# Performance work log

Measured on AMD Instinct MI355X. Metric: run time of the kernel, lower is better.

Reference implementation:

```python
import jax, jax.numpy as jnp
import numpy as np
from jax.scipy.special import gammaln

# NQ_IN + 4 == 2*H is required because the two kernel=1, padding=1 convs grow the
# length axis by 4 and the following nn.Linear(2H, H) acts on the length axis.
B, NQ_IN, NK, QDIM, KDIM, H = 16, 2044, 1024, 80, 256, 1024


def setup_inputs() -> dict:
    ks = jax.random.split(jax.random.key(0), 14)
    s = 0.02
    return {
        "query": jax.random.normal(ks[0], (B, NQ_IN, QDIM), jnp.float32),
        "key": jax.random.normal(ks[1], (B, NK, KDIM), jnp.float32),
        "query_lens": jnp.full((B,), 2 * H, jnp.int32),
        "key_lens": jnp.full((B,), NK, jnp.int32),
        # query branch params (Conv1d k=1 stored as (out,in); Linear as (out,in))
        "qc1_w": jax.random.normal(ks[2], (2 * H, QDIM), jnp.float32) * s,
        "qc1_b": jax.random.normal(ks[3], (2 * H,), jnp.float32) * s,
        "qc2_w": jax.random.normal(ks[4], (2 * H, 2 * H), jnp.float32) * s,
        "qc2_b": jax.random.normal(ks[5], (2 * H,), jnp.float32) * s,
        "ql_w": jax.random.normal(ks[6], (H, 2 * H), jnp.float32) * s,
        "ql_b": jax.random.normal(ks[7], (H,), jnp.float32) * s,
        # key branch params
        "kc_w": jax.random.normal(ks[8], (H, KDIM, 3), jnp.float32) * s,
        "kc_b": jax.random.normal(ks[9], (H,), jnp.float32) * s,
        "kl1_w": jax.random.normal(ks[10], (2 * H, H), jnp.float32) * s,
        "kl1_b": jax.random.normal(ks[11], (2 * H,), jnp.float32) * s,
        "kl2_w": jax.random.normal(ks[12], (H, 2 * H), jnp.float32) * s,
        "kl2_b": jax.random.normal(ks[13], (H,), jnp.float32) * s,
    }


def _log_beta_binom(query_lens, key_lens, tq, tk):
    # Standard MAS beta-binomial alignment prior over a (tq, tk) grid.
    i = jnp.arange(tq, dtype=jnp.float32)[None, :, None]
    j = jnp.arange(tk, dtype=jnp.float32)[None, None, :]
    ql = query_lens.astype(jnp.float32)[:, None, None]
    kl = key_lens.astype(jnp.float32)[:, None, None]
    a = i + 1.0
    b = jnp.maximum(ql - i, 1.0)
    n = jnp.maximum(kl - 1.0, 0.0)
    nmj = jnp.maximum(n - j, 0.0)

    def betaln(x, y):
        return gammaln(x) + gammaln(y) - gammaln(x + y)

    logp = (gammaln(n + 1.0) - gammaln(j + 1.0) - gammaln(nmj + 1.0)
            + betaln(j + a, nmj + b) - betaln(a, b))
    valid = (i < ql) & (j < kl)
    return jnp.where(valid, logp, -1e9)


def _forward(query, key, query_lens, key_lens,
             qc1_w, qc1_b, qc2_w, qc2_b, ql_w, ql_b,
             kc_w, kc_b, kl1_w, kl1_b, kl2_w, kl2_b):
    # query branch: b n c -> b c n, two k=1/p=1 convs (pad length, pointwise), Linear over LENGTH axis
    q = jnp.transpose(query, (0, 2, 1))                       # (B, QDIM, NQ_IN)
    q = jnp.pad(q, ((0, 0), (0, 0), (1, 1)))
    q = jnp.einsum('bcn,oc->bon', q, qc1_w) + qc1_b[None, :, None]   # (B, 2H, NQ_IN+2)
    q = jnp.pad(q, ((0, 0), (0, 0), (1, 1)))
    q = jnp.einsum('bcn,oc->bon', q, qc2_w) + qc2_b[None, :, None]   # (B, 2H, 2H)
    q = jnp.einsum('bcn,hn->bch', q, ql_w) + ql_b                    # (B, 2H, H) Linear on length axis

    # key branch: b n c -> b c n, Conv1d k=3 p=1, then two Linears over LENGTH axis
    k = jnp.transpose(key, (0, 2, 1))                         # (B, KDIM, NK)
    k = jax.lax.conv_general_dilated(k, kc_w, (1,), ((1, 1),),
                                     dimension_numbers=('NCH', 'OIH', 'NCH'))
    k = k + kc_b[None, :, None]                               # (B, H, NK=H)
    k = jnp.einsum('bcn,on->bco', k, kl1_w) + kl1_b           # (B, H, 2H)
    k = jnp.einsum('bco,ho->bch', k, kl2_w) + kl2_b           # (B, H, H)

    # dist = -cdist(q, k), computed via the GEMM form (same as torch.cdist mm mode)
    sq = (jnp.sum(q * q, -1)[:, :, None] + jnp.sum(k * k, -1)[:, None, :]
          - 2.0 * jnp.einsum('bnd,bmd->bnm', q, k))           # (B, 2H, H)
    dist = -jnp.sqrt(jnp.maximum(sq, 1e-12))

    prior = _log_beta_binom(query_lens, key_lens, q.shape[1], k.shape[1])
    return jax.nn.log_softmax(dist + prior, axis=-1)


def reference(query, key, query_lens, key_lens,
              qc1_w, qc1_b, qc2_w, qc2_b, ql_w, ql_b,
              kc_w, kc_b, kl1_w, kl1_b, kl2_w, kl2_b):
    return _forward(query, key, query_lens, key_lens,
                    qc1_w, qc1_b, qc2_w, qc2_b, ql_w, ql_b,
                    kc_w, kc_b, kl1_w, kl1_b, kl2_w, kl2_b)
```

## Files before the change

### kernel.cpp

```cpp
#include <hip/hip_runtime.h>
#include <math.h>

typedef unsigned short u16;
typedef float floatx4 __attribute__((ext_vector_type(4)));
typedef __bf16 bf16x8 __attribute__((ext_vector_type(8)));

#define BB   16
#define TQ   2048
#define TK   1024
#define HH   1024
#define H2   2048
#define QD   80
#define QDP  128
#define KD   256
#define NQ   2044
#define NKEY 1024
#define T12N 3072

__device__ __forceinline__ u16 f2bf(float f) {
  unsigned int u = __float_as_uint(f);
  u = u + 0x7fffu + ((u >> 16) & 1u);
  return (u16)(u >> 16);
}
__device__ __forceinline__ float bf2f(u16 s) {
  return __uint_as_float(((unsigned int)s) << 16);
}
__device__ __forceinline__ float tgf(const float* __restrict__ tbl, int x) {
  return tbl[(x < 8191) ? (x < 0 ? 0 : x) : 8191];
}

__global__ __launch_bounds__(256) void prep_all_k(
    const float* __restrict__ qc2_w, const float* __restrict__ kl2_w,
    const float* __restrict__ ql_w, const float* __restrict__ kc_w,
    const float* __restrict__ kl1_w,
    u16* __restrict__ qc2w, u16* __restrict__ kl2w, u16* __restrict__ qlw2,
    u16* __restrict__ kcp, float* __restrict__ colsum1, float* __restrict__ tbl)
{
  long b = blockIdx.x;
  const int t = threadIdx.x;
  __shared__ float red[256];
  if (b < 16384) {
    long i = b * 256 + t; qc2w[i] = f2bf(qc2_w[i]); return;
  }
  b -= 16384;
  if (b < 8192) {
    long i = b * 256 + t; kl2w[i] = f2bf(kl2_w[i]); return;
  }
  b -= 8192;
  if (b < 8192) {
    long i = b * 256 + t;
    int n = (int)(i & 2047);
    int h = (int)(i >> 11);
    qlw2[i] = (n < NQ) ? f2bf(ql_w[(long)h * H2 + n + 2]) : (u16)0; return;
  }
  b -= 8192;
  if (b < 3072) {
    long i = b * 256 + t;
    int r = (int)(i % 768);
    int o = (int)(i / 768);
    int tt = r >> 8, d = r & 255;
    kcp[i] = f2bf(kc_w[((long)o * KD + d) * 3 + tt]); return;
  }
  b -= 3072;
  if (b < 2048) {
    const float* row = kl1_w + b * (long)HH;
    float s = row[t] + row[t + 256] + row[t + 512] + row[t + 768];
    red[t] = s; __syncthreads();
    for (int st = 128; st > 0; st >>= 1) { if (t < st) red[t] += red[t + st]; __syncthreads(); }
    if (!t) colsum1[b] = red[0];
    return;
  }
  b -= 2048;
  { int i = (int)(b * 256 + t); if (i < 8192) tbl[i] = i ? (float)lgamma((double)i) : 0.0f; }
}

__global__ __launch_bounds__(256) void tpack_k(
    const float* __restrict__ kl1_w, const float* __restrict__ qc1_w,
    const float* __restrict__ query,
    u16* __restrict__ kl1T, u16* __restrict__ qc1T, u16* __restrict__ qT)
{
  __shared__ float tile[64][65];
  int bid = blockIdx.x;
  const int tid = threadIdx.x;
  const int r4 = tid >> 6, c = tid & 63;
  const float* src; u16* dst;
  int sr0, sc0, srcR, srcC, srcStride, dstC;
  if (bid < 512) {
    sr0 = (bid >> 4) * 64; sc0 = (bid & 15) * 64;
    src = kl1_w; srcR = 2048; srcC = 1024; srcStride = 1024;
    dst = kl1T; dstC = 2048;
  } else if ((bid -= 512) < 64) {
    sr0 = (bid >> 1) * 64; sc0 = (bid & 1) * 64;
    src = qc1_w; srcR = 2048; srcC = QD; srcStride = QD;
    dst = qc1T; dstC = 2048;
  } else {
    bid -= 64;
    const int b16 = bid >> 6, r = bid & 63;
    sr0 = (r >> 1) * 64; sc0 = (r & 1) * 64;
    src = query + (long)b16 * NQ * QD; srcR = NQ; srcC = QD; srcStride = QD;
    dst = qT + (long)b16 * QDP * 2048; dstC = 2048;
  }
#pragma unroll
  for (int rr = r4; rr < 64; rr += 4) {
    const int gr = sr0 + rr, gc = sc0 + c;
    tile[rr][c] = (gr < srcR && gc < srcC) ? src[(long)gr * srcStride + gc] : 0.f;
  }
  __syncthreads();
#pragma unroll
  for (int rr = r4; rr < 64; rr += 4)
    dst[(long)(sc0 + rr) * dstC + sr0 + c] = f2bf(tile[c][rr]);
}

__global__ __launch_bounds__(256) void pack_kcolT_k(const float* __restrict__ key, u16* __restrict__ out) {
  __shared__ float tile[64][65];
  const int bid = blockIdx.x, tid = threadIdx.x;
  const int b = bid >> 6, r = bid & 63;
  const int m0 = (r >> 2) * 64;
  const int d0 = (r & 3) * 64;
  const int r4 = tid >> 6, c = tid & 63;
#pragma unroll
  for (int rr = r4; rr < 64; rr += 4)
    tile[rr][c] = key[((long)b * NKEY + m0 + rr) * KD + d0 + c];
  __syncthreads();
#pragma unroll
  for (int t = 0; t < 3; t++) {
    const int n = m0 + 1 - t + c;
    if (n >= 0 && n < NKEY) {
#pragma unroll
      for (int rr = r4; rr < 64; rr += 4)
        out[((long)b * 768 + t * 256 + d0 + rr) * NKEY + n] = f2bf(tile[c][rr]);
    }
  }
  if (m0 == 0 && c == 0) {
#pragma unroll
    for (int rr = r4; rr < 64; rr += 4)
      out[((long)b * 768 + d0 + rr) * NKEY + 0] = (u16)0;
  }
  if (m0 == 960 && c == 0) {
#pragma unroll
    for (int rr = r4; rr < 64; rr += 4)
      out[((long)b * 768 + 512 + d0 + rr) * NKEY + (NKEY - 1)] = (u16)0;
  }
}

__global__ __launch_bounds__(256) void fold_bias_k(
    const float* __restrict__ qc2_w, const float* __restrict__ qc1_b, const float* __restrict__ qc2_b,
    const float* __restrict__ kl2_w, const float* __restrict__ kl1_b, const float* __restrict__ kl2_b,
    const float* __restrict__ ql_w, const float* __restrict__ colsum1,
    float* __restrict__ bqm, float* __restrict__ bkv, float* __restrict__ s1v, float* __restrict__ s0v,
    float* __restrict__ wsum)
{
  const int bid = blockIdx.x, t = threadIdx.x;
  float s = 0.f, s2 = 0.f;
  if (bid < H2) {
    const float* row = qc2_w + (long)bid * H2;
    for (int k = t; k < H2; k += 256) s += row[k] * qc1_b[k];
  } else if (bid < H2 + HH) {
    const float* row = kl2_w + (long)(bid - H2) * H2;
    for (int k = t; k < H2; k += 256) { const float rv = row[k]; s += rv * kl1_b[k]; s2 += rv * colsum1[k]; }
  } else {
    const float* row = ql_w + (long)(bid - H2 - HH) * H2;
    for (int m = 1 + t; m <= H2 - 2; m += 256) s += row[m];
  }
  __shared__ float red[256];
  __shared__ float red2[256];
  red[t] = s; red2[t] = s2; __syncthreads();
  for (int st = 128; st > 0; st >>= 1) {
    if (t < st) { red[t] += red[t + st]; red2[t] += red2[t + st]; }
    __syncthreads();
  }
  if (!t) {
    if (bid < H2) bqm[bid] = red[0] + qc2_b[bid];
    else if (bid < H2 + HH) { bkv[bid - H2] = red[0] + kl2_b[bid - H2]; wsum[bid - H2] = red2[0]; }
    else {
      int h = bid - H2 - HH;
      s1v[h] = red[0];
      s0v[h] = ql_w[(long)h * H2] + ql_w[(long)h * H2 + H2 - 1];
    }
  }
}

__device__ __forceinline__ void gld_lds16(const u16* g, u16* l) {
  __builtin_amdgcn_global_load_lds((const __attribute__((address_space(1))) void*)g,
                                   (__attribute__((address_space(3))) void*)l, 16, 0, 0);
}

template<int MODE>
__global__ __launch_bounds__(256) void gemm_bt(
    const u16* __restrict__ A, const u16* __restrict__ B, void* __restrict__ Cv,
    int M, int N, int K, int lda, int ldb, int swap, int kspl,
    long sA, long sB, long sC, long sN,
    const float* __restrict__ colb, const float* __restrict__ rowb,
    const float* __restrict__ r1m, const float* __restrict__ r1n,
    const float* __restrict__ r2m, const float* __restrict__ r2n,
    const float* __restrict__ c1p, const float* __restrict__ qnp,
    const float* __restrict__ knp, const float* __restrict__ crowp,
    const float* __restrict__ t12p,
    const int* __restrict__ qlensp, const int* __restrict__ klensp)
{
  __shared__ __align__(16) u16 As[128 * 32];
  __shared__ __align__(16) u16 Bs[128 * 32];
  const int bz = blockIdx.z;
  const int bb_ = (kspl > 1) ? bz / kspl : bz;
  const int ks_ = (kspl > 1) ? bz - bb_ * kspl : 0;
  const int tid  = threadIdx.x;
  const int lane = tid & 63;
  const int wv = tid >> 6;
  const int wm = ((tid >> 7) & 1) * 64;
  const int wn = ((tid >> 6) & 1) * 64;
  const int m0 = (swap ? blockIdx.x : blockIdx.y) * 128;
  const int n0 = (swap ? blockIdx.y : blockIdx.x) * 128;

  const int srow = wv * 32 + (lane >> 2);
  const int scol = (lane & 3) << 3;
  const u16* ga = A + bb_ * sA + (long)ks_ * K + (long)(m0 + srow) * lda + scol;
  const u16* gb = B + bb_ * sB + (long)ks_ * K + (long)(n0 + srow) * ldb + scol;
  u16* la0 = &As[(wv * 32) * 32];
  u16* la1 = &As[(wv * 32 + 16) * 32];
  u16* lb0 = &Bs[(wv * 32) * 32];
  u16* lb1 = &Bs[(wv * 32 + 16) * 32];
  const long a16 = (long)16 * lda;
  const long b16 = (long)16 * ldb;

  floatx4 acc[4][4];
#pragma unroll
  for (int a_ = 0; a_ < 4; a_++)
#pragma unroll
    for (int b_ = 0; b_ < 4; b_++) acc[a_][b_] = (floatx4){0.f, 0.f, 0.f, 0.f};

  const int fr = lane & 15;
  const int fk = (lane >> 4) << 3;

  for (int kb = 0; kb < K; kb += 32) {
    gld_lds16(ga,       la0);
    gld_lds16(ga + a16, la1);
    gld_lds16(gb,       lb0);
    gld_lds16(gb + b16, lb1);
    ga += 32; gb += 32;
    __syncthreads();
    bf16x8 af[4], bfr[4];
#pragma unroll
    for (int mi = 0; mi < 4; mi++)
      af[mi] = *reinterpret_cast<const bf16x8*>(&As[(wm + mi * 16 + fr) * 32 + fk]);
#pragma unroll
    for (int ni = 0; ni < 4; ni++)
      bfr[ni] = *reinterpret_cast<const bf16x8*>(&Bs[(wn + ni * 16 + fr) * 32 + fk]);
#pragma unroll
    for (int mi = 0; mi < 4; mi++)
#pragma unroll
      for (int ni = 0; ni < 4; ni++)
        acc[mi][ni] = __builtin_amdgcn_mfma_f32_16x16x32_bf16(af[mi], bfr[ni], acc[mi][ni], 0, 0, 0);
    __syncthreads();
  }

  const int fr4 = (lane >> 4) << 2;
  const int fc  = lane & 15;
  u16*   Cb16 = (u16*)Cv + (long)bz * sC;
  float* Cb32 = (float*)Cv + (long)bz * sC;
  const float* cbp  = colb ? colb + (long)bb_ * sN : nullptr;
  const float* r1np = r1n ? r1n + (long)bb_ * sN : nullptr;
  const float* r2np = r2n ? r2n + (long)bb_ * sN : nullptr;
  int qlv = 0, klv = 0;
  if (MODE == 2) { qlv = qlensp[bb_]; klv = klensp[bb_]; }
#pragma unroll
  for (int mi = 0; mi < 4; mi++) {
#pragma unroll
    for (int ni = 0; ni < 4; ni++) {
      const int gm0 = m0 + wm + mi * 16 + fr4;
      const int gn  = n0 + wn + ni * 16 + fc;
      const float cbv  = cbp ? cbp[gn] : 0.f;
      const float r1nv = r1np ? r1np[gn] : 0.f;
      const float r2nv = r2np ? r2np[gn] : 0.f;
      float knj = 0.f, c1j = 0.f;
      union { float4 v4; float a[4]; } qn4, cr4;
      if (MODE == 2) {
        knj = knp[(long)bb_ * TK + gn];
        c1j = c1p[(long)bb_ * TK + gn];
        qn4.v4 = *reinterpret_cast<const float4*>(qnp + (long)bb_ * TQ + gm0);
        cr4.v4 = *reinterpret_cast<const float4*>(crowp + (long)bb_ * TQ + gm0);
      }
#pragma unroll
      for (int rr = 0; rr < 4; rr++) {
        const int gm = gm0 + rr;
        float v = acc[mi][ni][rr] + cbv;
        if (rowb) v += rowb[gm];
        if (r1m)  v += r1m[gm] * r1nv;
        if (r2m)  v += r2m[gm] * r2nv;
        if (MODE == 2) {
          const float sq = fmaxf(qn4.a[rr] + knj - 2.0f * v, 1e-12f);
          const float dist = -sqrtf(sq);
          float res = -1e9f;
          if (gm < qlv && gn < klv)
            res = dist + cr4.a[rr] - c1j + t12p[(long)bb_ * T12N + gm + gn];
          Cb32[(long)gm * N + gn] = res;
        }
        else if (MODE == 1) Cb32[(long)gm * N + gn] = v;
        else                Cb16[(long)gm * N + gn] = f2bf(v);
      }
    }
  }
}

__global__ __launch_bounds__(256) void reduce_bk_k(const float* __restrict__ P, u16* __restrict__ out,
                                                   long chunk, int S, long total) {
  long j = ((long)blockIdx.x * 256 + threadIdx.x) * 4;
  if (j >= total) return;
  long b = j / chunk;
  const float* p = P + j + b * chunk * (S - 1);
  float4 s = *reinterpret_cast<const float4*>(p);
  for (int t = 1; t < S; t++) {
    const float4 v = *reinterpret_cast<const float4*>(p + (long)t * chunk);
    s.x += v.x; s.y += v.y; s.z += v.z; s.w += v.w;
  }
  union { u16 h[4]; uint2 u; } o;
  o.h[0] = f2bf(s.x); o.h[1] = f2bf(s.y); o.h[2] = f2bf(s.z); o.h[3] = f2bf(s.w);
  *reinterpret_cast<uint2*>(out + j) = o.u;
}

__global__ __launch_bounds__(256) void u_k(
    const u16* __restrict__ TpT, const float* __restrict__ qlb,
    const float* __restrict__ s1, const float* __restrict__ s0,
    const float* __restrict__ tbl, const int* __restrict__ qlens, const int* __restrict__ klens,
    float* __restrict__ u0, float* __restrict__ u1, float* __restrict__ u2,
    float* __restrict__ sc, float* __restrict__ c1,
    float* __restrict__ crow, float* __restrict__ t12)
{
  const int bid = blockIdx.x, t = threadIdx.x;
  __shared__ float4 red[256];
  if (bid < BB * QDP) {
    uint2 v = reinterpret_cast<const uint2*>(TpT + (long)bid * HH)[t];
    float a0 = bf2f((u16)(v.x & 0xffff)), a1 = bf2f((u16)(v.x >> 16));
    float a2 = bf2f((u16)(v.y & 0xffff)), a3 = bf2f((u16)(v.y >> 16));
    float4 q  = reinterpret_cast<const float4*>(qlb)[t];
    float4 w1 = reinterpret_cast<const float4*>(s1)[t];
    float4 w0 = reinterpret_cast<const float4*>(s0)[t];
    float4 s;
    s.x = a0 * q.x  + a1 * q.y  + a2 * q.z  + a3 * q.w;
    s.y = a0 * w1.x + a1 * w1.y + a2 * w1.z + a3 * w1.w;
    s.z = a0 * w0.x + a1 * w0.y + a2 * w0.z + a3 * w0.w;
    s.w = 0.f;
    red[t] = s; __syncthreads();
    for (int st = 128; st > 0; st >>= 1) {
      if (t < st) { red[t].x += red[t + st].x; red[t].y += red[t + st].y; red[t].z += red[t + st].z; }
      __syncthreads();
    }
    if (!t) { u0[bid] = red[0].x; u1[bid] = red[0].y; u2[bid] = red[0].z; }
  } else if (bid < BB * QDP + 6) {
    const int idx = bid - BB * QDP;
    const float* X = (idx == 1 || idx == 5) ? s1 : (idx == 2) ? s0 : qlb;
    const float* Y = (idx == 1 || idx == 3) ? s1 : (idx == 0) ? qlb : s0;
    float4 x = reinterpret_cast<const float4*>(X)[t];
    float4 y = reinterpret_cast<const float4*>(Y)[t];
    float4 s; s.x = x.x * y.x + x.y * y.y + x.z * y.z + x.w * y.w; s.y = s.z = s.w = 0.f;
    red[t] = s; __syncthreads();
    for (int st = 128; st > 0; st >>= 1) {
      if (t < st) red[t].x += red[t + st].x;
      __syncthreads();
    }
    if (!t) sc[idx] = red[0].x;
  } else if (bid < BB * QDP + 6 + 64) {
    const int idx = bid - (BB * QDP + 6);
    const int b = idx >> 2;
    const int j = ((idx & 3) << 8) | t;
    const int kl = klens[b];
    const int n_ = (kl - 1 > 0) ? kl - 1 : 0;
    c1[b * TK + j] = tgf(tbl, j + 1) + tgf(tbl, n_ - j + 1);
  } else if (bid < BB * QDP + 6 + 64 + 128) {
    const int idx = bid - (BB * QDP + 6 + 64);
    const int b = idx >> 3;
    const int i = ((idx & 7) << 8) | t;
    const int ql = qlens[b], kl = klens[b];
    const int n_ = (kl - 1 > 0) ? kl - 1 : 0;
    const int bb = (ql - i > 1) ? ql - i : 1;
    crow[b * TQ + i] = tgf(tbl, n_ + 1) + tgf(tbl, i + 1 + bb) - tgf(tbl, i + 1)
                     - tgf(tbl, bb) - tgf(tbl, i + 1 + n_ + bb);
  } else {
    const int idx = bid - (BB * QDP + 6 + 64 + 128);
    const int b = idx / 12;
    const int s = (idx - b * 12) * 256 + t;
    const int ql = qlens[b], kl = klens[b];
    const int n_ = (kl - 1 > 0) ? kl - 1 : 0;
    t12[b * T12N + s] = tgf(tbl, s + 1) + tgf(tbl, n_ + ql - s);
  }
}

__global__ __launch_bounds__(256) void qn_k(
    const u16* __restrict__ Wq, const float* __restrict__ WqG,
    const float* __restrict__ u0, const float* __restrict__ u1, const float* __restrict__ u2,
    const float* __restrict__ bqm, const float* __restrict__ qc2_b,
    const float* __restrict__ sc, float* __restrict__ qn)
{
  const int bx = blockIdx.x, t = threadIdx.x;
  const int b = bx >> 10;
  const int i = ((bx & 1023) << 1) | (t >> 7);
  const int d = t & 127;
  const float w  = bf2f(Wq[(long)i * QDP + d]);
  const float g  = WqG[((long)b * H2 + i) * QDP + d];
  const float bq = bqm[i], q2 = qc2_b[i];
  const float uu = u0[b * QDP + d] + bq * u1[b * QDP + d] + q2 * u2[b * QDP + d];
  __shared__ float red[256];
  red[t] = w * (g + 2.f * uu); __syncthreads();
  for (int s = 64; s > 0; s >>= 1) { if ((t & 127) < s) red[t] += red[t + s]; __syncthreads(); }
  if (d == 0) {
    const float cst = sc[0] + bq * bq * sc[1] + q2 * q2 * sc[2]
                    + 2.f * (bq * sc[3] + q2 * sc[4] + bq * q2 * sc[5]);
    qn[b * TQ + i] = red[t] + cst;
  }
}

__global__ __launch_bounds__(256) void rownormk_k(
    const u16* __restrict__ K3, const float* __restrict__ qlb,
    const float* __restrict__ s1, const float* __restrict__ s0,
    float* __restrict__ kn, float* __restrict__ yb, float* __restrict__ y1, float* __restrict__ y0)
{
  const long r = blockIdx.x;
  const int t = threadIdx.x;
  uint2 v = reinterpret_cast<const uint2*>(K3 + r * HH)[t];
  float a0 = bf2f((u16)(v.x & 0xffff)), a1 = bf2f((u16)(v.x >> 16));
  float a2 = bf2f((u16)(v.y & 0xffff)), a3 = bf2f((u16)(v.y >> 16));
  float4 q  = reinterpret_cast<const float4*>(qlb)[t];
  float4 w1 = reinterpret_cast<const float4*>(s1)[t];
  float4 w0 = reinterpret_cast<const float4*>(s0)[t];
  float4 s;
  s.x = a0 * a0   + a1 * a1   + a2 * a2   + a3 * a3;
  s.y = a0 * q.x  + a1 * q.y  + a2 * q.z  + a3 * q.w;
  s.z = a0 * w1.x + a1 * w1.y + a2 * w1.z + a3 * w1.w;
  s.w = a0 * w0.x + a1 * w0.y + a2 * w0.z + a3 * w0.w;
  __shared__ float4 red[256];
  red[t] = s; __syncthreads();
  for (int st = 128; st > 0; st >>= 1) {
    if (t < st) {
      red[t].x += red[t + st].x; red[t].y += red[t + st].y;
      red[t].z += red[t + st].z; red[t].w += red[t + st].w;
    }
    __syncthreads();
  }
  if (!t) { kn[r] = red[0].x; yb[r] = red[0].y; y1[r] = red[0].z; y0[r] = red[0].w; }
}

__global__ __launch_bounds__(256) void finalize_k(float* __restrict__ out)
{
  const int i = blockIdx.x;
  const int b = blockIdx.y;
  const int tid = threadIdx.x;
  const long rowoff = ((long)b * TQ + i) * TK;
  float4 v = *reinterpret_cast<const float4*>(out + rowoff + (tid << 2));
  float m = fmaxf(fmaxf(v.x, v.y), fmaxf(v.z, v.w));
#pragma unroll
  for (int k = 1; k < 64; k <<= 1) m = fmaxf(m, __shfl_xor(m, k, 64));
  __shared__ float wred[8];
  if ((tid & 63) == 0) wred[tid >> 6] = m;
  __syncthreads();
  const float gmax = fmaxf(fmaxf(wred[0], wred[1]), fmaxf(wred[2], wred[3]));
  const float L2E = 1.4426950408889634f;
  float ls = exp2f((v.x - gmax) * L2E) + exp2f((v.y - gmax) * L2E)
           + exp2f((v.z - gmax) * L2E) + exp2f((v.w - gmax) * L2E);
#pragma unroll
  for (int k = 1; k < 64; k <<= 1) ls += __shfl_xor(ls, k, 64);
  if ((tid & 63) == 0) wred[4 + (tid >> 6)] = ls;
  __syncthreads();
  const float tot = (wred[4] + wred[5]) + (wred[6] + wred[7]);
  const float lse = gmax + logf(tot);
  v.x -= lse; v.y -= lse; v.z -= lse; v.w -= lse;
  *reinterpret_cast<float4*>(out + rowoff + (tid << 2)) = v;
}

extern "C" void kernel_launch(void* const* d_in, const int* in_sizes, int n_in,
                              void* d_out, int out_size, void* d_ws, size_t ws_size,
                              hipStream_t stream)
{
  (void)in_sizes; (void)n_in; (void)out_size; (void)ws_size;
  const float* query = (const float*)d_in[0];
  const float* key   = (const float*)d_in[1];
  const int*   qlens = (const int*)d_in[2];
  const int*   klens = (const int*)d_in[3];
  const float* qc1_w = (const float*)d_in[4];
  const float* qc1_b = (const float*)d_in[5];
  const float* qc2_w = (const float*)d_in[6];
  const float* qc2_b = (const float*)d_in[7];
  const float* ql_w  = (const float*)d_in[8];
  const float* ql_b  = (const float*)d_in[9];
  const float* kc_w  = (const float*)d_in[10];
  const float* kc_b  = (const float*)d_in[11];
  const float* kl1_w = (const float*)d_in[12];
  const float* kl1_b = (const float*)d_in[13];
  const float* kl2_w = (const float*)d_in[14];
  const float* kl2_b = (const float*)d_in[15];

  size_t off = 0;
  char* ws = (char*)d_ws;
  auto alloc = [&](size_t bytes) -> char* {
    char* p = ws + off; off += (bytes + 255) & ~(size_t)255; return p;
  };
  u16* qc2w_bf = (u16*)alloc(2ull * H2 * H2);
  u16* qc1T_bf = (u16*)alloc(2ull * QDP * H2);
  u16* kl2w_bf = (u16*)alloc(2ull * HH * H2);
  u16* kl1T_bf = (u16*)alloc(2ull * HH * H2);
  u16* qT_bf   = (u16*)alloc(2ull * BB * QDP * 2048);
  u16* kcolT_bf= (u16*)d_ws;
  u16* Z2_bf   = (u16*)d_ws;
  u16* qlw2_bf = (u16*)alloc(2ull * HH * 2048);
  u16* kcp_bf  = (u16*)alloc(2ull * HH * 768);
  u16* TpT_bf  = (u16*)alloc(2ull * H2 * HH);
  char* pool   = alloc(2ull * BB * HH * NKEY);
  float* Pbuf  = (float*)pool;
  u16* X_bf    = (u16*)pool;
  float* tbl  = (float*)alloc(4ull * 8192);
  u16* Wq_bf  = (u16*)alloc(2ull * H2 * QDP);
  u16* Wk_bf  = (u16*)alloc(2ull * HH * NKEY);
  float* bqm  = (float*)alloc(4ull * H2);
  float* bkv  = (float*)alloc(4ull * HH);
  float* s1v  = (float*)alloc(4ull * HH);
  float* s0v  = (float*)alloc(4ull * HH);
  float* wsum = (float*)alloc(4ull * HH);
  float* colsum1 = (float*)alloc(4ull * H2);
  u16* K3_bf  = (u16*)alloc(2ull * BB * TK * HH);
  float* qnv  = (float*)alloc(4ull * BB * TQ);
  float* knv  = (float*)alloc(4ull * BB * TK);
  float* ybv  = (float*)alloc(4ull * BB * TK);
  float* y1v  = (float*)alloc(4ull * BB * TK);
  float* y0v  = (float*)alloc(4ull * BB * TK);
  float* u0v  = (float*)alloc(4ull * BB * QDP);
  float* u1v  = (float*)alloc(4ull * BB * QDP);
  float* u2v  = (float*)alloc(4ull * BB * QDP);
  float* c1v  = (float*)alloc(4ull * BB * TK);
  float* crowv= (float*)alloc(4ull * BB * TQ);
  float* t12v = (float*)alloc(4ull * BB * T12N);
  float* scv  = (float*)alloc(256);
  float* WqG  = (float*)d_out;
  u16* G_bf   = (u16*)((char*)d_out + 16777216);

  prep_all_k<<<37920, 256, 0, stream>>>(qc2_w, kl2_w, ql_w, kc_w, kl1_w,
                                        qc2w_bf, kl2w_bf, qlw2_bf, kcp_bf, colsum1, tbl);
  tpack_k<<<1600, 256, 0, stream>>>(kl1_w, qc1_w, query, kl1T_bf, qc1T_bf, qT_bf);
  fold_bias_k<<<4096, 256, 0, stream>>>(qc2_w, qc1_b, qc2_b, kl2_w, kl1_b, kl2_b, ql_w, colsum1,
                                        bqm, bkv, s1v, s0v, wsum);

  gemm_bt<1><<<dim3(1, 16, 16), 256, 0, stream>>>(qc2w_bf, qc1T_bf, Pbuf, H2, QDP, 128,
      H2, H2, 0, 16, 0, 0, (long)H2 * QDP, 0,
      nullptr, nullptr, nullptr, nullptr, nullptr, nullptr,
      nullptr, nullptr, nullptr, nullptr, nullptr, nullptr, nullptr);
  reduce_bk_k<<<256, 256, 0, stream>>>(Pbuf, Wq_bf, (long)H2 * QDP, 16, (long)H2 * QDP);

  gemm_bt<1><<<dim3(8, 8, 8), 256, 0, stream>>>(kl2w_bf, kl1T_bf, Pbuf, HH, NKEY, 256,
      H2, H2, 0, 8, 0, 0, (long)HH * NKEY, 0,
      nullptr, nullptr, nullptr, nullptr, nullptr, nullptr,
      nullptr, nullptr, nullptr, nullptr, nullptr, nullptr, nullptr);
  reduce_bk_k<<<1024, 256, 0, stream>>>(Pbuf, Wk_bf, (long)HH * NKEY, 8, (long)HH * NKEY);

  gemm_bt<1><<<dim3(8, 16, 4), 256, 0, stream>>>(qT_bf, qlw2_bf, Pbuf, H2, HH, 512,
      2048, 2048, 0, 4, 0, 0, (long)H2 * HH, 0,
      nullptr, nullptr, nullptr, nullptr, nullptr, nullptr,
      nullptr, nullptr, nullptr, nullptr, nullptr, nullptr, nullptr);
  reduce_bk_k<<<2048, 256, 0, stream>>>(Pbuf, TpT_bf, (long)H2 * HH, 4, (long)H2 * HH);

  gemm_bt<1><<<dim3(1, 1, 128), 256, 0, stream>>>(TpT_bf, TpT_bf, Pbuf, 128, 128, 128,
      HH, HH, 0, 8, (long)QDP * HH, (long)QDP * HH, 128 * 128, 0,
      nullptr, nullptr, nullptr, nullptr, nullptr, nullptr,
      nullptr, nullptr, nullptr, nullptr, nullptr, nullptr, nullptr);
  reduce_bk_k<<<256, 256, 0, stream>>>(Pbuf, G_bf, 128 * 128, 8, (long)BB * 128 * 128);

  gemm_bt<1><<<dim3(1, 16, 16), 256, 0, stream>>>(Wq_bf, G_bf, WqG, H2, QDP, QDP,
      QDP, QDP, 0, 1, 0, (long)QDP * QDP, (long)H2 * QDP, 0,
      nullptr, nullptr, nullptr, nullptr, nullptr, nullptr,
      nullptr, nullptr, nullptr, nullptr, nullptr, nullptr, nullptr);
  u_k<<<BB * QDP + 6 + 64 + 128 + 192, 256, 0, stream>>>(TpT_bf, ql_b, s1v, s0v, tbl, qlens, klens,
                                                         u0v, u1v, u2v, scv, c1v, crowv, t12v);
  qn_k<<<BB * TQ / 2, 256, 0, stream>>>(Wq_bf, WqG, u0v, u1v, u2v, bqm, qc2_b, scv, qnv);

  pack_kcolT_k<<<1024, 256, 0, stream>>>(key, kcolT_bf);
  gemm_bt<0><<<dim3(6, 8, BB), 256, 0, stream>>>(Wk_bf, kcolT_bf, X_bf, HH, 768, NKEY,
      NKEY, NKEY, 0, 1, 0, (long)768 * NKEY, (long)HH * 768, 0,
      nullptr, nullptr, nullptr, nullptr, nullptr, nullptr,
      nullptr, nullptr, nullptr, nullptr, nullptr, nullptr, nullptr);
  gemm_bt<0><<<dim3(8, 8, BB), 256, 0, stream>>>(kcp_bf, X_bf, K3_bf, HH, NKEY, 768,
      768, 768, 1, 1, 0, (long)HH * 768, (long)TK * HH, 0,
      bkv, nullptr, kc_b, wsum, nullptr, nullptr,
      nullptr, nullptr, nullptr, nullptr, nullptr, nullptr, nullptr);

  gemm_bt<1><<<dim3(8, 1, 32), 256, 0, stream>>>(K3_bf, TpT_bf, Pbuf, TK, QDP, 512,
      HH, HH, 1, 2, (long)TK * HH, (long)QDP * HH, (long)TK * QDP, 0,
      nullptr, nullptr, nullptr, nullptr, nullptr, nullptr,
      nullptr, nullptr, nullptr, nullptr, nullptr, nullptr, nullptr);
  reduce_bk_k<<<2048, 256, 0, stream>>>(Pbuf, Z2_bf, (long)TK * QDP, 2, (long)BB * TK * QDP);

  rownormk_k<<<BB * TK, 256, 0, stream>>>(K3_bf, ql_b, s1v, s0v, knv, ybv, y1v, y0v);

  gemm_bt<2><<<dim3(8, 16, BB), 256, 0, stream>>>(Wq_bf, Z2_bf, (float*)d_out, H2, TK, QDP,
      QDP, QDP, 0, 1, 0, (long)TK * QDP, (long)TQ * TK, (long)TK,
      ybv, nullptr, bqm, y1v, qc2_b, y0v,
      c1v, qnv, knv, crowv, t12v, qlens, klens);

  finalize_k<<<dim3(TQ, BB, 1), 256, 0, stream>>>((float*)d_out);
}
```

Measured before the change: 650.9 us.

## Fuse distance GEMM with log-softmax using two-pass recompute in one kernel

Replaces the final MFMA GEMM epilogue kernel plus the separate row log-softmax pass with one kernel. Each block owns 128 query rows and computes the K=128 GEMM twice: first to accumulate an online max/sum-exp per row, then to write normalized outputs staged through LDS for coalesced float4 stores. This removes writing the 128MB fp32 intermediate and reading it back, at the cost of doubling the small GEMM. The grid is now only 256 blocks of 512 threads, so occupancy and parallelism are reduced.

After: 616.8 us. -5.2%, faster.

```diff
diff --git a/kernel.cpp b/kernel.cpp
--- a/kernel.cpp
+++ b/kernel.cpp
@@ -185,18 +185,14 @@
                                    (__attribute__((address_space(3))) void*)l, 16, 0, 0);
 }
 
-template<int MODE>
+template<int OUTF32>
 __global__ __launch_bounds__(256) void gemm_bt(
     const u16* __restrict__ A, const u16* __restrict__ B, void* __restrict__ Cv,
     int M, int N, int K, int lda, int ldb, int swap, int kspl,
     long sA, long sB, long sC, long sN,
     const float* __restrict__ colb, const float* __restrict__ rowb,
     const float* __restrict__ r1m, const float* __restrict__ r1n,
-    const float* __restrict__ r2m, const float* __restrict__ r2n,
-    const float* __restrict__ c1p, const float* __restrict__ qnp,
-    const float* __restrict__ knp, const float* __restrict__ crowp,
-    const float* __restrict__ t12p,
-    const int* __restrict__ qlensp, const int* __restrict__ klensp)
+    const float* __restrict__ r2m, const float* __restrict__ r2n)
 {
   __shared__ __align__(16) u16 As[128 * 32];
   __shared__ __align__(16) u16 Bs[128 * 32];
@@ -260,8 +256,6 @@
   const float* cbp  = colb ? colb + (long)bb_ * sN : nullptr;
   const float* r1np = r1n ? r1n + (long)bb_ * sN : nullptr;
   const float* r2np = r2n ? r2n + (long)bb_ * sN : nullptr;
-  int qlv = 0, klv = 0;
-  if (MODE == 2) { qlv = qlensp[bb_]; klv = klensp[bb_]; }
 #pragma unroll
   for (int mi = 0; mi < 4; mi++) {
 #pragma unroll
@@ -271,14 +265,6 @@
       const float cbv  = cbp ? cbp[gn] : 0.f;
       const float r1nv = r1np ? r1np[gn] : 0.f;
       const float r2nv = r2np ? r2np[gn] : 0.f;
-      float knj = 0.f, c1j = 0.f;
-      union { float4 v4; float a[4]; } qn4, cr4;
-      if (MODE == 2) {
-        knj = knp[(long)bb_ * TK + gn];
-        c1j = c1p[(long)bb_ * TK + gn];
-        qn4.v4 = *reinterpret_cast<const float4*>(qnp + (long)bb_ * TQ + gm0);
-        cr4.v4 = *reinterpret_cast<const float4*>(crowp + (long)bb_ * TQ + gm0);
-      }
 #pragma unroll
       for (int rr = 0; rr < 4; rr++) {
         const int gm = gm0 + rr;
@@ -286,16 +272,8 @@
         if (rowb) v += rowb[gm];
         if (r1m)  v += r1m[gm] * r1nv;
         if (r2m)  v += r2m[gm] * r2nv;
-        if (MODE == 2) {
-          const float sq = fmaxf(qn4.a[rr] + knj - 2.0f * v, 1e-12f);
-          const float dist = -sqrtf(sq);
-          float res = -1e9f;
-          if (gm < qlv && gn < klv)
-            res = dist + cr4.a[rr] - c1j + t12p[(long)bb_ * T12N + gm + gn];
-          Cb32[(long)gm * N + gn] = res;
-        }
-        else if (MODE == 1) Cb32[(long)gm * N + gn] = v;
-        else                Cb16[(long)gm * N + gn] = f2bf(v);
+        if (OUTF32) Cb32[(long)gm * N + gn] = v;
+        else        Cb16[(long)gm * N + gn] = f2bf(v);
       }
     }
   }
@@ -438,31 +416,175 @@
   if (!t) { kn[r] = red[0].x; yb[r] = red[0].y; y1[r] = red[0].z; y0[r] = red[0].w; }
 }
 
-__global__ __launch_bounds__(256) void finalize_k(float* __restrict__ out)
-{
-  const int i = blockIdx.x;
-  const int b = blockIdx.y;
-  const int tid = threadIdx.x;
-  const long rowoff = ((long)b * TQ + i) * TK;
-  float4 v = *reinterpret_cast<const float4*>(out + rowoff + (tid << 2));
-  float m = fmaxf(fmaxf(v.x, v.y), fmaxf(v.z, v.w));
-#pragma unroll
-  for (int k = 1; k < 64; k <<= 1) m = fmaxf(m, __shfl_xor(m, k, 64));
-  __shared__ float wred[8];
-  if ((tid & 63) == 0) wred[tid >> 6] = m;
+#define L2E 1.4426950408889634f
+__global__ __launch_bounds__(512) void smax_k(
+    const u16* __restrict__ Wq, const u16* __restrict__ Z2, float* __restrict__ out,
+    const float* __restrict__ ybv, const float* __restrict__ y1v, const float* __restrict__ y0v,
+    const float* __restrict__ bqmv, const float* __restrict__ qc2_b,
+    const float* __restrict__ qnv, const float* __restrict__ knv, const float* __restrict__ c1v,
+    const float* __restrict__ crowv, const float* __restrict__ t12v,
+    const int* __restrict__ qlens, const int* __restrict__ klens)
+{
+  __shared__ float vst[64][132];
+  __shared__ float t12s[1152];
+  __shared__ float qns[128], crs[128], bqms[128], q2bs[128];
+  __shared__ float2 lseb[4][128];
+  __shared__ float lsef[128];
+
+  const int mt = blockIdx.x, b = blockIdx.y;
+  const int m0 = mt * 128;
+  const int t = threadIdx.x;
+  const int w = t >> 6, lane = t & 63;
+  const int wm2 = (w >> 2) * 64, wn2 = (w & 3) * 32;
+  const int fr = lane & 15, fk = (lane >> 4) << 3;
+  const int fr4 = (lane >> 4) << 2, fc = lane & 15;
+  const int qlv = qlens[b], klv = klens[b];
+  const int h = w >> 2;
+
+  if (t < 128) {
+    qns[t]  = qnv[(long)b * TQ + m0 + t];
+    crs[t]  = crowv[(long)b * TQ + m0 + t];
+    bqms[t] = bqmv[m0 + t];
+    q2bs[t] = qc2_b[m0 + t];
+  }
+  for (int k = t; k < 1152; k += 512) t12s[k] = t12v[(long)b * T12N + m0 + k];
+
+  bf16x8 af[4][4];
+#pragma unroll
+  for (int kc = 0; kc < 4; kc++)
+#pragma unroll
+    for (int mi = 0; mi < 4; mi++)
+      af[kc][mi] = *reinterpret_cast<const bf16x8*>(
+          Wq + (long)(m0 + wm2 + mi * 16 + fr) * QDP + kc * 32 + fk);
+
+  const u16* Zb = Z2 + (long)b * TK * QDP;
+  const float* ybp = ybv + (long)b * TK;
+  const float* y1p = y1v + (long)b * TK;
+  const float* y0p = y0v + (long)b * TK;
+  const float* knp = knv + (long)b * TK;
+  const float* c1p = c1v + (long)b * TK;
+  float* outp = out + (long)b * TQ * TK + (long)m0 * TK;
+
+  float m_[16], s_[16];
+#pragma unroll
+  for (int ri = 0; ri < 16; ri++) { m_[ri] = -3.0e38f; s_[ri] = 0.f; }
+
   __syncthreads();
-  const float gmax = fmaxf(fmaxf(wred[0], wred[1]), fmaxf(wred[2], wred[3]));
-  const float L2E = 1.4426950408889634f;
-  float ls = exp2f((v.x - gmax) * L2E) + exp2f((v.y - gmax) * L2E)
-           + exp2f((v.z - gmax) * L2E) + exp2f((v.w - gmax) * L2E);
-#pragma unroll
-  for (int k = 1; k < 64; k <<= 1) ls += __shfl_xor(ls, k, 64);
-  if ((tid & 63) == 0) wred[4 + (tid >> 6)] = ls;
-  __syncthreads();
-  const float tot = (wred[4] + wred[5]) + (wred[6] + wred[7]);
-  const float lse = gmax + logf(tot);
-  v.x -= lse; v.y -= lse; v.z -= lse; v.w -= lse;
-  *reinterpret_cast<float4*>(out + rowoff + (tid << 2)) = v;
+
+  for (int pass = 0; pass < 2; pass++) {
+    for (int nt = 0; nt < 8; nt++) {
+      bf16x8 bfr[4][2];
+#pragma unroll
+      for (int kc = 0; kc < 4; kc++)
+#pragma unroll
+        for (int nj = 0; nj < 2; nj++)
+          bfr[kc][nj] = *reinterpret_cast<const bf16x8*>(
+              Zb + (long)(nt * 128 + wn2 + nj * 16 + fr) * QDP + kc * 32 + fk);
+
+      floatx4 acc[4][2];
+#pragma unroll
+      for (int mi = 0; mi < 4; mi++)
+#pragma unroll
+        for (int nj = 0; nj < 2; nj++) acc[mi][nj] = (floatx4){0.f, 0.f, 0.f, 0.f};
+#pragma unroll
+      for (int kc = 0; kc < 4; kc++)
+#pragma unroll
+        for (int mi = 0; mi < 4; mi++)
+#pragma unroll
+          for (int nj = 0; nj < 2; nj++)
+            acc[mi][nj] = __builtin_amdgcn_mfma_f32_16x16x32_bf16(af[kc][mi], bfr[kc][nj], acc[mi][nj], 0, 0, 0);
+
+      int gj[2]; float ybj[2], y1j[2], y0j[2], knj[2], c1j[2];
+#pragma unroll
+      for (int nj = 0; nj < 2; nj++) {
+        gj[nj]  = nt * 128 + wn2 + nj * 16 + fc;
+        ybj[nj] = ybp[gj[nj]]; y1j[nj] = y1p[gj[nj]]; y0j[nj] = y0p[gj[nj]];
+        knj[nj] = knp[gj[nj]]; c1j[nj] = c1p[gj[nj]];
+      }
+
+#pragma unroll
+      for (int mi = 0; mi < 4; mi++) {
+#pragma unroll
+        for (int rr = 0; rr < 4; rr++) {
+          const int rl = wm2 + mi * 16 + fr4 + rr;
+          const float qnr = qns[rl], crr = crs[rl], bqr = bqms[rl], q2r = q2bs[rl];
+          float vv[2];
+#pragma unroll
+          for (int nj = 0; nj < 2; nj++) {
+            const float Sv = acc[mi][nj][rr] + ybj[nj] + bqr * y1j[nj] + q2r * y0j[nj];
+            const float sq = fmaxf(qnr + knj[nj] - 2.0f * Sv, 1e-12f);
+            const float x = -__builtin_amdgcn_sqrtf(sq) + crr - c1j[nj] + t12s[rl + gj[nj]];
+            vv[nj] = ((m0 + rl) < qlv && gj[nj] < klv) ? x : -1e9f;
+          }
+          const int ri = mi * 4 + rr;
+          if (pass == 0) {
+            const float nm = fmaxf(m_[ri], fmaxf(vv[0], vv[1]));
+            s_[ri] = s_[ri] * exp2f((m_[ri] - nm) * L2E)
+                   + exp2f((vv[0] - nm) * L2E) + exp2f((vv[1] - nm) * L2E);
+            m_[ri] = nm;
+          } else {
+            const float l = lsef[rl];
+            acc[mi][0][rr] = vv[0] - l;
+            acc[mi][1][rr] = vv[1] - l;
+          }
+        }
+      }
+
+      if (pass == 1) {
+#pragma unroll
+        for (int hh = 0; hh < 2; hh++) {
+          if (h == hh) {
+#pragma unroll
+            for (int mi = 0; mi < 4; mi++)
+#pragma unroll
+              for (int nj = 0; nj < 2; nj++)
+#pragma unroll
+                for (int rr = 0; rr < 4; rr++)
+                  vst[mi * 16 + fr4 + rr][wn2 + nj * 16 + fc] = acc[mi][nj][rr];
+          }
+          __syncthreads();
+#pragma unroll
+          for (int k = 0; k < 4; k++) {
+            const int fi = k * 512 + t;
+            const int row = fi >> 5, lc4 = (fi & 31) << 2;
+            *reinterpret_cast<float4*>(outp + (long)(hh * 64 + row) * TK + nt * 128 + lc4) =
+                *reinterpret_cast<const float4*>(&vst[row][lc4]);
+          }
+          __syncthreads();
+        }
+      }
+    }
+
+    if (pass == 0) {
+#pragma unroll
+      for (int k2 = 1; k2 <= 8; k2 <<= 1) {
+#pragma unroll
+        for (int ri = 0; ri < 16; ri++) {
+          const float om = __shfl_xor(m_[ri], k2, 64);
+          const float os = __shfl_xor(s_[ri], k2, 64);
+          const float nm = fmaxf(m_[ri], om);
+          s_[ri] = s_[ri] * exp2f((m_[ri] - nm) * L2E) + os * exp2f((om - nm) * L2E);
+          m_[ri] = nm;
+        }
+      }
+      if (fc == 0) {
+#pragma unroll
+        for (int mi = 0; mi < 4; mi++)
+#pragma unroll
+          for (int rr = 0; rr < 4; rr++)
+            lseb[w & 3][wm2 + mi * 16 + fr4 + rr] = make_float2(m_[mi * 4 + rr], s_[mi * 4 + rr]);
+      }
+      __syncthreads();
+      if (t < 128) {
+        const float2 e0 = lseb[0][t], e1 = lseb[1][t], e2 = lseb[2][t], e3 = lseb[3][t];
+        const float mm = fmaxf(fmaxf(e0.x, e1.x), fmaxf(e2.x, e3.x));
+        const float ss = e0.y * exp2f((e0.x - mm) * L2E) + e1.y * exp2f((e1.x - mm) * L2E)
+                       + e2.y * exp2f((e2.x - mm) * L2E) + e3.y * exp2f((e3.x - mm) * L2E);
+        lsef[t] = mm + logf(ss);
+      }
+      __syncthreads();
+    }
+  }
 }
 
 extern "C" void kernel_launch(void* const* d_in, const int* in_sizes, int n_in,
@@ -538,32 +660,27 @@
 
   gemm_bt<1><<<dim3(1, 16, 16), 256, 0, stream>>>(qc2w_bf, qc1T_bf, Pbuf, H2, QDP, 128,
       H2, H2, 0, 16, 0, 0, (long)H2 * QDP, 0,
-      nullptr, nullptr, nullptr, nullptr, nullptr, nullptr,
-      nullptr, nullptr, nullptr, nullptr, nullptr, nullptr, nullptr);
+      nullptr, nullptr, nullptr, nullptr, nullptr, nullptr);
   reduce_bk_k<<<256, 256, 0, stream>>>(Pbuf, Wq_bf, (long)H2 * QDP, 16, (long)H2 * QDP);
 
   gemm_bt<1><<<dim3(8, 8, 8), 256, 0, stream>>>(kl2w_bf, kl1T_bf, Pbuf, HH, NKEY, 256,
       H2, H2, 0, 8, 0, 0, (long)HH * NKEY, 0,
-      nullptr, nullptr, nullptr, nullptr, nullptr, nullptr,
-      nullptr, nullptr, nullptr, nullptr, nullptr, nullptr, nullptr);
+      nullptr, nullptr, nullptr, nullptr, nullptr, nullptr);
   reduce_bk_k<<<1024, 256, 0, stream>>>(Pbuf, Wk_bf, (long)HH * NKEY, 8, (long)HH * NKEY);
 
   gemm_bt<1><<<dim3(8, 16, 4), 256, 0, stream>>>(qT_bf, qlw2_bf, Pbuf, H2, HH, 512,
       2048, 2048, 0, 4, 0, 0, (long)H2 * HH, 0,
-      nullptr, nullptr, nullptr, nullptr, nullptr, nullptr,
-      nullptr, nullptr, nullptr, nullptr, nullptr, nullptr, nullptr);
+      nullptr, nullptr, nullptr, nullptr, nullptr, nullptr);
   reduce_bk_k<<<2048, 256, 0, stream>>>(Pbuf, TpT_bf, (long)H2 * HH, 4, (long)H2 * HH);
 
   gemm_bt<1><<<dim3(1, 1, 128), 256, 0, stream>>>(TpT_bf, TpT_bf, Pbuf, 128, 128, 128,
       HH, HH, 0, 8, (long)QDP * HH, (long)QDP * HH, 128 * 128, 0,
-      nullptr, nullptr, nullptr, nullptr, nullptr, nullptr,
-      nullptr, nullptr, nullptr, nullptr, nullptr, nullptr, nullptr);
+      nullptr, nullptr, nullptr, nullptr, nullptr, nullptr);
   reduce_bk_k<<<256, 256, 0, stream>>>(Pbuf, G_bf, 128 * 128, 8, (long)BB * 128 * 128);
 
   gemm_bt<1><<<dim3(1, 16, 16), 256, 0, stream>>>(Wq_bf, G_bf, WqG, H2, QDP, QDP,
       QDP, QDP, 0, 1, 0, (long)QDP * QDP, (long)H2 * QDP, 0,
-      nullptr, nullptr, nullptr, nullptr, nullptr, nullptr,
-      nullptr, nullptr, nullptr, nullptr, nullptr, nullptr, nullptr);
+      nullptr, nullptr, nullptr, nullptr, nullptr, nullptr);
   u_k<<<BB * QDP + 6 + 64 + 128 + 192, 256, 0, stream>>>(TpT_bf, ql_b, s1v, s0v, tbl, qlens, klens,
                                                          u0v, u1v, u2v, scv, c1v, crowv, t12v);
   qn_k<<<BB * TQ / 2, 256, 0, stream>>>(Wq_bf, WqG, u0v, u1v, u2v, bqm, qc2_b, scv, qnv);
@@ -571,25 +688,18 @@
   pack_kcolT_k<<<1024, 256, 0, stream>>>(key, kcolT_bf);
   gemm_bt<0><<<dim3(6, 8, BB), 256, 0, stream>>>(Wk_bf, kcolT_bf, X_bf, HH, 768, NKEY,
       NKEY, NKEY, 0, 1, 0, (long)768 * NKEY, (long)HH * 768, 0,
-      nullptr, nullptr, nullptr, nullptr, nullptr, nullptr,
-      nullptr, nullptr, nullptr, nullptr, nullptr, nullptr, nullptr);
+      nullptr, nullptr, nullptr, nullptr, nullptr, nullptr);
   gemm_bt<0><<<dim3(8, 8, BB), 256, 0, stream>>>(kcp_bf, X_bf, K3_bf, HH, NKEY, 768,
       768, 768, 1, 1, 0, (long)HH * 768, (long)TK * HH, 0,
-      bkv, nullptr, kc_b, wsum, nullptr, nullptr,
-      nullptr, nullptr, nullptr, nullptr, nullptr, nullptr, nullptr);
+      bkv, nullptr, kc_b, wsum, nullptr, nullptr);
 
   gemm_bt<1><<<dim3(8, 1, 32), 256, 0, stream>>>(K3_bf, TpT_bf, Pbuf, TK, QDP, 512,
       HH, HH, 1, 2, (long)TK * HH, (long)QDP * HH, (long)TK * QDP, 0,
-      nullptr, nullptr, nullptr, nullptr, nullptr, nullptr,
-      nullptr, nullptr, nullptr, nullptr, nullptr, nullptr, nullptr);
+      nullptr, nullptr, nullptr, nullptr, nullptr, nullptr);
   reduce_bk_k<<<2048, 256, 0, stream>>>(Pbuf, Z2_bf, (long)TK * QDP, 2, (long)BB * TK * QDP);
 
   rownormk_k<<<BB * TK, 256, 0, stream>>>(K3_bf, ql_b, s1v, s0v, knv, ybv, y1v, y0v);
 
-  gemm_bt<2><<<dim3(8, 16, BB), 256, 0, stream>>>(Wq_bf, Z2_bf, (float*)d_out, H2, TK, QDP,
-      QDP, QDP, 0, 1, 0, (long)TK * QDP, (long)TQ * TK, (long)TK,
-      ybv, nullptr, bqm, y1v, qc2_b, y0v,
-      c1v, qnv, knv, crowv, t12v, qlens, klens);
-
-  finalize_k<<<dim3(TQ, BB, 1), 256, 0, stream>>>((float*)d_out);
-}
+  smax_k<<<dim3(16, 16), 512, 0, stream>>>(Wq_bf, Z2_bf, (float*)d_out,
+      ybv, y1v, y0v, bqm, qc2_b, qnv, knv, c1v, crowv, t12v, qlens, klens);
+}
```
